# Optimization experiments

Measured on AMD Instinct MI355X. Metric: run time of the kernel, lower is better.

The kernel has to match this reference:

```python
import jax, jax.numpy as jnp
import numpy as np

EPS = 1e-5
POW = 0.5

def _eig_fun(X, fn):
    # symmetric matrix function via eigendecomposition: V f(diag) V^T
    w, V = jnp.linalg.eigh(X)
    return jnp.einsum('...ij,...j,...kj->...ik', V, fn(w), V)

def sym_pow(X, p):
    return _eig_fun(X, lambda w: jnp.power(w, p))

def sym_log(X):
    return _eig_fun(X, jnp.log)

def sym_exp(X):
    return _eig_fun(X, jnp.exp)

def exp_at(T, G):
    # Riemannian exp of tangent T at base point G (affine-invariant metric)
    Gh = sym_pow(G, 0.5)
    Gnh = sym_pow(G, -0.5)
    return Gh @ sym_exp(Gnh @ T @ Gnh) @ Gh

def bary_geom(X, n_iter=1):
    # Karcher/geodesic mean of batch of SPD matrices X: (B, n, n)
    # init at arithmetic mean, n_iter Karcher flow steps
    G = jnp.mean(X, axis=0)
    for _ in range(n_iter):
        Gh = sym_pow(G, 0.5)
        Gnh = sym_pow(G, -0.5)
        T = jnp.mean(sym_log(Gnh @ X @ Gnh), axis=0)
        G = Gh @ sym_exp(T) @ Gh
    return G

def setup_inputs() -> dict:
    key = jax.random.key(0)
    N, h, n = 256, 16, 64
    k1, k2, k3 = jax.random.split(key, 3)
    A = jax.random.normal(k1, (N, h, n, n), dtype=jnp.float32)
    # well-conditioned SPD inputs with distinct eigenvalues
    X = A @ jnp.swapaxes(A, -1, -2) / n + 0.5 * jnp.eye(n, dtype=jnp.float32)
    Bw = jax.random.normal(k2, (n, n), dtype=jnp.float32) * 0.1
    weight = sym_exp(0.5 * (Bw + Bw.T))  # SPD parameter near identity
    Bm = jax.random.normal(k3, (n, n), dtype=jnp.float32) * 0.1
    M = sym_exp(0.5 * (Bm + Bm.T))       # SPD deformation parameter
    shift = jnp.ones((1,), dtype=jnp.float32)
    return {"X": X, "weight": weight, "M": M, "shift": shift}

def reference(X, weight, M, shift):
    N, h, n, _ = X.shape
    Xb = X.reshape(N * h, n, n)
    Xp = sym_pow(Xb, POW)                  # PowerEig(X, po)
    Mnh = sym_pow(M, -0.5)
    Mh = sym_pow(M, 0.5)
    Xc = Mnh @ Xp @ Mnh                    # CongrG(., M, 'neg')
    Wp = sym_pow(weight, POW)              # PowerEig(weight, po)
    Wc = Mnh @ Wp @ Mnh                    # CongrG1(weight, M, 'neg')

    mean = bary_geom(Xc)                   # BaryGeom (training path)
    mnh = sym_pow(mean, -0.5)
    # pal1(mean, LogG(Xc, mean)) = PT of Riemannian log to identity
    T = sym_log(mnh @ Xc @ mnh)            # (N*h, n, n) tangent at I
    # cal_var: mean squared Riemannian distance to the mean
    var = jnp.mean(jnp.sum(T * T, axis=(-2, -1)))
    T = T * (shift[0] / jnp.sqrt(var + EPS))  # scale1
    Wh = sym_pow(weight, 0.5)
    S = Wh @ T @ Wh                        # pal2(weight, LogG1(.))
    Y = exp_at(S, Wc)                      # ExpG(., weight_deformed)
    Y = Mh @ Y @ Mh                        # CongrG(., M, 'pos')
    Y = sym_pow(Y, 1.0 / POW)              # PowerEig(., 1/po)
    return Y.reshape(N, h, n, n)
```

## Files before the change

### kernel.cpp

```cpp
#include <hip/hip_runtime.h>
#include <math.h>

#define PITCH 72
#define SW_BATCH 9
#define SW_SMALL 10
#define NPART 32
#define EPS2_ROT 1e-12f

#define OFF_ACCG 0
#define OFF_ACCT (NPART*4096)
#define OFF_BASE (2*NPART*4096)
#define SL_MNH  (OFF_BASE + 0*4096)
#define SL_MH   (OFF_BASE + 1*4096)
#define SL_WH   (OFF_BASE + 2*4096)
#define SL_P    (OFF_BASE + 3*4096)
#define SL_Q    (OFF_BASE + 4*4096)
#define SL_GH   (OFF_BASE + 5*4096)
#define SL_GNH  (OFF_BASE + 6*4096)
#define SL_MNH2 (OFF_BASE + 7*4096)
#define SL_WCH  (OFF_BASE + 8*4096)
#define OFF_VAR (OFF_BASE + 9*4096)
#define SL_SC   (OFF_BASE + 9*4096 + 1)

struct __align__(16) F4 { float v[4]; };

struct __align__(16) Smem {
  float S0[64*PITCH];
  float S1[64*PITCH];
  float w2[64];
  float wc[64];
  float nrm[64];
  float red[256];
  int flag;
};

__device__ __forceinline__ void g2s(float* dst, const float* __restrict__ src) {
  int t = threadIdx.x;
#pragma unroll
  for (int i = 0; i < 4; ++i) {
    int e4 = t + (i << 8);
    F4 vv = *(const F4*)&src[e4 * 4];
    *(F4*)&dst[(e4 >> 4) * PITCH + (e4 & 15) * 4] = vv;
  }
  __syncthreads();
}
__device__ __forceinline__ void g2s_scaled(float* dst, const float* __restrict__ src, float sc) {
  int t = threadIdx.x;
#pragma unroll
  for (int i = 0; i < 4; ++i) {
    int e4 = t + (i << 8);
    F4 vv = *(const F4*)&src[e4 * 4];
#pragma unroll
    for (int m = 0; m < 4; ++m) vv.v[m] *= sc;
    *(F4*)&dst[(e4 >> 4) * PITCH + (e4 & 15) * 4] = vv;
  }
  __syncthreads();
}
__device__ __forceinline__ void s2g(float* __restrict__ dst, const float* src) {
  int t = threadIdx.x;
#pragma unroll
  for (int i = 0; i < 4; ++i) {
    int e4 = t + (i << 8);
    F4 vv = *(const F4*)&src[(e4 >> 4) * PITCH + (e4 & 15) * 4];
    *(F4*)&dst[e4 * 4] = vv;
  }
  __syncthreads();
}

template<int MODE>
__device__ void mmX(Smem& sm) {
  int t = threadIdx.x;
  int R0 = t >> 4;
  if (MODE == 2) {
    int J0 = t & 15;
    float acc[4][4] = {};
    for (int kb = 0; kb < 64; kb += 4) {
      F4 a4[4];
#pragma unroll
      for (int i = 0; i < 4; ++i)
        a4[i] = *(const F4*)&sm.S0[(R0 + 16 * i) * PITCH + kb];
#pragma unroll
      for (int kk = 0; kk < 4; ++kk) {
        float b[4];
#pragma unroll
        for (int m = 0; m < 4; ++m) b[m] = sm.S1[(J0 + 16 * m) * PITCH + kb + kk];
#pragma unroll
        for (int i = 0; i < 4; ++i)
#pragma unroll
          for (int m = 0; m < 4; ++m) acc[i][m] = fmaf(a4[i].v[kk], b[m], acc[i][m]);
      }
    }
    __syncthreads();
#pragma unroll
    for (int i = 0; i < 4; ++i)
#pragma unroll
      for (int m = 0; m < 4; ++m)
        sm.S0[(R0 + 16 * i) * PITCH + J0 + 16 * m] = acc[i][m];
    __syncthreads();
  } else {
    int J = (t & 15) * 4;
    float acc[4][4] = {};
    for (int kb = 0; kb < 64; kb += 4) {
      F4 a4[4], b4[4];
#pragma unroll
      for (int i = 0; i < 4; ++i) {
        const float* L = (MODE == 0 || MODE == 3) ? sm.S1 : sm.S0;
        a4[i] = *(const F4*)&L[(R0 + 16 * i) * PITCH + kb];
      }
#pragma unroll
      for (int kk = 0; kk < 4; ++kk) {
        const float* Rp = (MODE == 0) ? sm.S0 : sm.S1;
        b4[kk] = *(const F4*)&Rp[(kb + kk) * PITCH + J];
      }
#pragma unroll
      for (int i = 0; i < 4; ++i)
#pragma unroll
        for (int kk = 0; kk < 4; ++kk)
#pragma unroll
          for (int m = 0; m < 4; ++m)
            acc[i][m] = fmaf(a4[i].v[kk], b4[kk].v[m], acc[i][m]);
    }
    __syncthreads();
#pragma unroll
    for (int i = 0; i < 4; ++i) {
      F4 o;
#pragma unroll
      for (int m = 0; m < 4; ++m) o.v[m] = acc[i][m];
      *(F4*)&sm.S0[(R0 + 16 * i) * PITCH + J] = o;
    }
    __syncthreads();
  }
}

__device__ void reconT(Smem& sm) {
  __syncthreads();
  int t = threadIdx.x;
  int R0 = t >> 4;
  int J = (t & 15) * 4;
  float acc[4][4] = {};
  for (int k = 0; k < 64; ++k) {
    float w = sm.wc[k];
    float a[4];
#pragma unroll
    for (int i = 0; i < 4; ++i) a[i] = w * sm.S0[k * PITCH + R0 + 16 * i];
    F4 b = *(const F4*)&sm.S0[k * PITCH + J];
#pragma unroll
    for (int i = 0; i < 4; ++i)
#pragma unroll
      for (int m = 0; m < 4; ++m) acc[i][m] = fmaf(a[i], b.v[m], acc[i][m]);
  }
#pragma unroll
  for (int i = 0; i < 4; ++i) {
    F4 o;
#pragma unroll
    for (int m = 0; m < 4; ++m) o.v[m] = acc[i][m];
    *(F4*)&sm.S1[(R0 + 16 * i) * PITCH + J] = o;
  }
  __syncthreads();
}

__device__ float frob2(Smem& sm) {
  int t = threadIdx.x;
  float s = 0.f;
#pragma unroll
  for (int i = 0; i < 4; ++i) {
    int e4 = t + (i << 8);
    F4 vv = *(const F4*)&sm.S0[(e4 >> 4) * PITCH + (e4 & 15) * 4];
#pragma unroll
    for (int m = 0; m < 4; ++m) s = fmaf(vv.v[m], vv.v[m], s);
  }
  sm.red[t] = s;
  __syncthreads();
  for (int o = 128; o; o >>= 1) { if (t < o) sm.red[t] += sm.red[t + o]; __syncthreads(); }
  float f = sm.red[0];
  __syncthreads();
  return f;
}

__device__ void hestenes(Smem& sm, int sweeps) {
  const int t = threadIdx.x;
  const int g = t >> 3;
  const int u = t & 7;
  float* A = sm.S0;

  {
    float sa = 0.f, sb = 0.f;
#pragma unroll
    for (int i = 0; i < 8; ++i) {
      float va = A[g * PITCH + u + 8 * i];
      float vb = A[(g + 32) * PITCH + u + 8 * i];
      sa = fmaf(va, va, sa); sb = fmaf(vb, vb, sb);
    }
    sa += __shfl_xor(sa, 1); sa += __shfl_xor(sa, 2); sa += __shfl_xor(sa, 4);
    sb += __shfl_xor(sb, 1); sb += __shfl_xor(sb, 2); sb += __shfl_xor(sb, 4);
    if (u == 0) { sm.nrm[g] = sa; sm.nrm[g + 32] = sb; }
    if (t == 0) sm.flag = 0;
  }
  __syncthreads();

  for (int s = 0; s < sweeps; ++s) {
    for (int r = 0; r < 63; ++r) {
      int p, q;
      if (g == 0) { p = 63; q = r; }
      else {
        int a = r + g;      if (a >= 63) a -= 63;
        int b = r + 63 - g; if (b >= 63) b -= 63;
        p = a; q = b;
      }
      const int bp = p * PITCH + u, bq = q * PITCH + u;
      float cp[8], cq[8];
#pragma unroll
      for (int i = 0; i < 8; ++i) { cp[i] = A[bp + 8 * i]; cq[i] = A[bq + 8 * i]; }
      float d = 0.f;
#pragma unroll
      for (int i = 0; i < 8; ++i) d = fmaf(cp[i], cq[i], d);
      d += __shfl_xor(d, 1); d += __shfl_xor(d, 2); d += __shfl_xor(d, 4);
      float dpp = sm.nrm[p], dqq = sm.nrm[q];
      if (d * d > EPS2_ROT * (dpp * dqq)) {
        float tau = (dqq - dpp) * (0.5f * __builtin_amdgcn_rcpf(d));
        float tt = __builtin_amdgcn_rcpf(fabsf(tau) +
                                         __builtin_amdgcn_sqrtf(fmaf(tau, tau, 1.f)));
        if (tau < 0.f) tt = -tt;
        float c = __builtin_amdgcn_rsqf(fmaf(tt, tt, 1.f));
        float s_ = tt * c;
#pragma unroll
        for (int i = 0; i < 8; ++i) {
          A[bp + 8 * i] = c * cp[i] - s_ * cq[i];
          A[bq + 8 * i] = s_ * cp[i] + c * cq[i];
        }
        if (u == 0) {
          float td = tt * d;
          sm.nrm[p] = dpp - td;
          sm.nrm[q] = dqq + td;
          sm.flag = 1;
        }
      }
      __syncthreads();
    }
    int f = sm.flag;
    __syncthreads();
    if (f == 0) break;
    if (t == 0) sm.flag = 0;
    __syncthreads();
  }

  {
    float sa = 0.f, sb = 0.f;
#pragma unroll
    for (int i = 0; i < 8; ++i) {
      float va = A[g * PITCH + u + 8 * i];
      float vb = A[(g + 32) * PITCH + u + 8 * i];
      sa = fmaf(va, va, sa); sb = fmaf(vb, vb, sb);
    }
    sa += __shfl_xor(sa, 1); sa += __shfl_xor(sa, 2); sa += __shfl_xor(sa, 4);
    sb += __shfl_xor(sb, 1); sb += __shfl_xor(sb, 2); sb += __shfl_xor(sb, 4);
    if (u == 0) { sm.w2[g] = sa; sm.w2[g + 32] = sb; }
  }
  __syncthreads();
}


__global__ __launch_bounds__(256) void kzero(float* ws) {
  int i = blockIdx.x * 256 + threadIdx.x;
  if (i < OFF_BASE) ws[i] = 0.f;
  if (i == 0) ws[OFF_VAR] = 0.f;
}

__global__ __launch_bounds__(256, 4) void kprep(const float* __restrict__ weight,
                                                const float* __restrict__ M,
                                                float* ws) {
  __shared__ Smem sm;
  int t = threadIdx.x;
  g2s(sm.S0, M);
  hestenes(sm, SW_SMALL);
  if (t < 64) sm.wc[t] = powf(fmaxf(sm.w2[t], 1e-12f), -1.25f);
  reconT(sm); s2g(ws + SL_MNH, sm.S1);
  if (t < 64) sm.wc[t] = powf(fmaxf(sm.w2[t], 1e-12f), -0.75f);
  reconT(sm); s2g(ws + SL_MH, sm.S1);

  g2s(sm.S0, weight);
  hestenes(sm, SW_SMALL);
  if (t < 64) sm.wc[t] = powf(fmaxf(sm.w2[t], 1e-12f), -0.75f);
  reconT(sm); s2g(ws + SL_WH, sm.S1);

  g2s(sm.S0, ws + SL_MNH);
  mmX<1>(sm);
  g2s(sm.S1, ws + SL_MNH);
  mmX<1>(sm);
  hestenes(sm, SW_SMALL);
  if (t < 64) sm.wc[t] = powf(fmaxf(sm.w2[t], 1e-12f), -0.75f);
  reconT(sm); s2g(ws + SL_WCH, sm.S1);
  if (t < 64) sm.wc[t] = powf(fmaxf(sm.w2[t], 1e-12f), -1.25f);
  reconT(sm);
  g2s(sm.S0, ws + SL_WH);
  mmX<0>(sm);
  s2g(ws + SL_P, sm.S0);
  g2s(sm.S0, ws + SL_WCH);
  g2s(sm.S1, ws + SL_MH);
  mmX<0>(sm);
  s2g(ws + SL_Q, sm.S0);
}

__global__ __launch_bounds__(256, 4) void k1(const float* __restrict__ X,
                                             float* __restrict__ out, float* ws) {
  __shared__ Smem sm;
  int t = threadIdx.x;
  size_t b = blockIdx.x;
  g2s(sm.S0, X + b * 4096);
  hestenes(sm, SW_BATCH);
  g2s(sm.S1, ws + SL_MNH);
  mmX<1>(sm);
  if (t < 64) sm.wc[t] = powf(fmaxf(sm.w2[t], 1e-12f), -0.75f);
  reconT(sm);
  float* Xc = out + b * 4096;
  float* acc = ws + OFF_ACCG + (size_t)(blockIdx.x & (NPART - 1)) * 4096;
#pragma unroll
  for (int i = 0; i < 4; ++i) {
    int e4 = t + (i << 8);
    F4 vv = *(const F4*)&sm.S1[(e4 >> 4) * PITCH + (e4 & 15) * 4];
    *(F4*)&Xc[e4 * 4] = vv;
#pragma unroll
    for (int m = 0; m < 4; ++m) atomicAdd(acc + e4 * 4 + m, vv.v[m]);
  }
}

__global__ __launch_bounds__(256, 4) void ksmall2(float* ws, float invB) {
  __shared__ Smem sm;
  int t = threadIdx.x;
#pragma unroll
  for (int i = 0; i < 4; ++i) {
    int e4 = t + (i << 8);
    F4 sum = {{0.f, 0.f, 0.f, 0.f}};
    for (int p = 0; p < NPART; ++p) {
      F4 vv = *(const F4*)&ws[OFF_ACCG + p * 4096 + e4 * 4];
#pragma unroll
      for (int m = 0; m < 4; ++m) sum.v[m] += vv.v[m];
    }
#pragma unroll
    for (int m = 0; m < 4; ++m) sum.v[m] *= invB;
    *(F4*)&sm.S0[(e4 >> 4) * PITCH + (e4 & 15) * 4] = sum;
  }
  __syncthreads();
  hestenes(sm, SW_SMALL);
  if (t < 64) sm.wc[t] = powf(fmaxf(sm.w2[t], 1e-12f), -0.75f);
  reconT(sm); s2g(ws + SL_GH, sm.S1);
  if (t < 64) sm.wc[t] = powf(fmaxf(sm.w2[t], 1e-12f), -1.25f);
  reconT(sm); s2g(ws + SL_GNH, sm.S1);
}

__global__ __launch_bounds__(256, 4) void k2(const float* __restrict__ XcBuf, float* ws) {
  __shared__ Smem sm;
  int t = threadIdx.x;
  size_t b = blockIdx.x;
  g2s(sm.S0, XcBuf + b * 4096);
  g2s(sm.S1, ws + SL_GNH);
  mmX<1>(sm);
  mmX<0>(sm);
  hestenes(sm, SW_BATCH);
  if (t < 64) {
    float s2 = fmaxf(sm.w2[t], 1e-12f);
    sm.wc[t] = 0.5f * logf(s2) / s2;
  }
  reconT(sm);
  float* acc = ws + OFF_ACCT + (size_t)(blockIdx.x & (NPART - 1)) * 4096;
#pragma unroll
  for (int i = 0; i < 4; ++i) {
    int e4 = t + (i << 8);
    F4 vv = *(const F4*)&sm.S1[(e4 >> 4) * PITCH + (e4 & 15) * 4];
#pragma unroll
    for (int m = 0; m < 4; ++m) atomicAdd(acc + e4 * 4 + m, vv.v[m]);
  }
}

__global__ __launch_bounds__(256, 4) void ksmall3(float* ws, float invB) {
  __shared__ Smem sm;
  int t = threadIdx.x;
#pragma unroll
  for (int i = 0; i < 4; ++i) {
    int e4 = t + (i << 8);
    F4 sum = {{0.f, 0.f, 0.f, 0.f}};
    for (int p = 0; p < NPART; ++p) {
      F4 vv = *(const F4*)&ws[OFF_ACCT + p * 4096 + e4 * 4];
#pragma unroll
      for (int m = 0; m < 4; ++m) sum.v[m] += vv.v[m];
    }
#pragma unroll
    for (int m = 0; m < 4; ++m) sum.v[m] *= invB;
    *(F4*)&sm.S0[(e4 >> 4) * PITCH + (e4 & 15) * 4] = sum;
  }
  __syncthreads();
  float mu = sqrtf(frob2(sm)) + 1e-3f;
  if (t < 64) sm.S0[t * PITCH + t] += mu;
  __syncthreads();
  hestenes(sm, SW_SMALL);
  if (t < 64) {
    float s2 = fmaxf(sm.w2[t], 1e-12f);
    sm.wc[t] = expf(sqrtf(s2) - mu) / s2;
  }
  reconT(sm);
  g2s(sm.S0, ws + SL_GH);
  mmX<1>(sm);
  g2s(sm.S1, ws + SL_GH);
  mmX<1>(sm);
  hestenes(sm, SW_SMALL);
  if (t < 64) sm.wc[t] = powf(fmaxf(sm.w2[t], 1e-12f), -1.25f);
  reconT(sm); s2g(ws + SL_MNH2, sm.S1);
}

__global__ __launch_bounds__(256, 4) void k3(float* __restrict__ buf, float* ws) {
  __shared__ Smem sm;
  int t = threadIdx.x;
  size_t b = blockIdx.x;
  g2s(sm.S0, buf + b * 4096);
  g2s(sm.S1, ws + SL_MNH2);
  mmX<1>(sm);
  mmX<0>(sm);
  hestenes(sm, SW_BATCH);
  if (t < 64) {
    float s2 = fmaxf(sm.w2[t], 1e-12f);
    sm.wc[t] = 0.5f * logf(s2) / s2;
  }
  reconT(sm);
  float ssq = 0.f;
  float* Tg = buf + b * 4096;
#pragma unroll
  for (int i = 0; i < 4; ++i) {
    int e4 = t + (i << 8);
    F4 vv = *(const F4*)&sm.S1[(e4 >> 4) * PITCH + (e4 & 15) * 4];
    *(F4*)&Tg[e4 * 4] = vv;
#pragma unroll
    for (int m = 0; m < 4; ++m) ssq = fmaf(vv.v[m], vv.v[m], ssq);
  }
  sm.red[t] = ssq;
  __syncthreads();
  for (int o = 128; o; o >>= 1) { if (t < o) sm.red[t] += sm.red[t + o]; __syncthreads(); }
  if (t == 0) atomicAdd(ws + OFF_VAR, sm.red[0]);
}

__global__ void kscale(float* ws, const float* __restrict__ shift, float invB) {
  if (threadIdx.x == 0 && blockIdx.x == 0) {
    float var = ws[OFF_VAR] * invB;
    ws[SL_SC] = shift[0] / sqrtf(var + 1e-5f);
  }
}

__global__ __launch_bounds__(256, 4) void k4(float* __restrict__ buf, float* ws) {
  __shared__ Smem sm;
  int t = threadIdx.x;
  size_t b = blockIdx.x;
  float sc = ws[SL_SC];
  g2s_scaled(sm.S0, buf + b * 4096, sc);
  g2s(sm.S1, ws + SL_P);
  mmX<0>(sm);
  mmX<2>(sm);
  float mu = sqrtf(frob2(sm)) + 1e-3f;
  if (t < 64) sm.S0[t * PITCH + t] += mu;
  __syncthreads();
  hestenes(sm, SW_BATCH);
  if (t < 64) {
    float s2 = fmaxf(sm.w2[t], 1e-12f);
    sm.wc[t] = expf(sqrtf(s2) - mu) / s2;
  }
  g2s(sm.S1, ws + SL_Q);
  mmX<2>(sm);
  reconT(sm);
  mmX<3>(sm);
  s2g(buf + b * 4096, sm.S0);
}

extern "C" void kernel_launch(void* const* d_in, const int* in_sizes, int n_in,
                              void* d_out, int out_size, void* d_ws, size_t ws_size,
                              hipStream_t stream) {
  const float* X      = (const float*)d_in[0];
  const float* weight = (const float*)d_in[1];
  const float* M      = (const float*)d_in[2];
  const float* shift  = (const float*)d_in[3];
  float* out = (float*)d_out;
  float* ws  = (float*)d_ws;
  int B = in_sizes[0] / 4096;
  float invB = 1.f / (float)B;

  hipLaunchKernelGGL(kzero,   dim3(OFF_BASE / 256), dim3(256), 0, stream, ws);
  hipLaunchKernelGGL(kprep,   dim3(1), dim3(256), 0, stream, weight, M, ws);
  hipLaunchKernelGGL(k1,      dim3(B), dim3(256), 0, stream, X, out, ws);
  hipLaunchKernelGGL(ksmall2, dim3(1), dim3(256), 0, stream, ws, invB);
  hipLaunchKernelGGL(k2,      dim3(B), dim3(256), 0, stream, out, ws);
  hipLaunchKernelGGL(ksmall3, dim3(1), dim3(256), 0, stream, ws, invB);
  hipLaunchKernelGGL(k3,      dim3(B), dim3(256), 0, stream, out, ws);
  hipLaunchKernelGGL(kscale,  dim3(1), dim3(64), 0, stream, ws, shift, invB);
  hipLaunchKernelGGL(k4,      dim3(B), dim3(256), 0, stream, out, ws);
}
```

Before: 9.694 ms.

## Run one-sided Jacobi per wavefront in registers, four matrices per block

Replaces the block-wide shared-memory Hestenes Jacobi with a register-resident version. Each 64-lane wavefront owns one matrix, one column per lane, and exchanges columns with xor shuffles in a round-robin pairing, so the per-rotation __syncthreads and LDS traffic go away. Each block now processes four matrices, and the batched kernels (k1-k4) are relaunched with B/4 blocks and a smaller shared pitch. The cost is heavy register pressure (64+64 floats per lane, occupancy hint lowered to 3), fewer blocks, and a higher sweep cap (12 vs 9) that may add iterations before convergence.

After: 9.168 ms. 5.4% less time.

```diff
diff --git a/kernel.cpp b/kernel.cpp
--- a/kernel.cpp
+++ b/kernel.cpp
@@ -2,7 +2,8 @@
 #include <math.h>
 
 #define PITCH 72
-#define SW_BATCH 9
+#define NP 68
+#define SW_BATCH 12
 #define SW_SMALL 10
 #define NPART 32
 #define EPS2_ROT 1e-12f
@@ -44,18 +45,6 @@
   }
   __syncthreads();
 }
-__device__ __forceinline__ void g2s_scaled(float* dst, const float* __restrict__ src, float sc) {
-  int t = threadIdx.x;
-#pragma unroll
-  for (int i = 0; i < 4; ++i) {
-    int e4 = t + (i << 8);
-    F4 vv = *(const F4*)&src[e4 * 4];
-#pragma unroll
-    for (int m = 0; m < 4; ++m) vv.v[m] *= sc;
-    *(F4*)&dst[(e4 >> 4) * PITCH + (e4 & 15) * 4] = vv;
-  }
-  __syncthreads();
-}
 __device__ __forceinline__ void s2g(float* __restrict__ dst, const float* src) {
   int t = threadIdx.x;
 #pragma unroll
@@ -71,65 +60,37 @@
 __device__ void mmX(Smem& sm) {
   int t = threadIdx.x;
   int R0 = t >> 4;
-  if (MODE == 2) {
-    int J0 = t & 15;
-    float acc[4][4] = {};
-    for (int kb = 0; kb < 64; kb += 4) {
-      F4 a4[4];
-#pragma unroll
-      for (int i = 0; i < 4; ++i)
-        a4[i] = *(const F4*)&sm.S0[(R0 + 16 * i) * PITCH + kb];
-#pragma unroll
-      for (int kk = 0; kk < 4; ++kk) {
-        float b[4];
-#pragma unroll
-        for (int m = 0; m < 4; ++m) b[m] = sm.S1[(J0 + 16 * m) * PITCH + kb + kk];
-#pragma unroll
-        for (int i = 0; i < 4; ++i)
-#pragma unroll
-          for (int m = 0; m < 4; ++m) acc[i][m] = fmaf(a4[i].v[kk], b[m], acc[i][m]);
-      }
-    }
-    __syncthreads();
+  int J = (t & 15) * 4;
+  float acc[4][4] = {};
+  for (int kb = 0; kb < 64; kb += 4) {
+    F4 a4[4], b4[4];
+#pragma unroll
+    for (int i = 0; i < 4; ++i) {
+      const float* L = (MODE == 0) ? sm.S1 : sm.S0;
+      a4[i] = *(const F4*)&L[(R0 + 16 * i) * PITCH + kb];
+    }
+#pragma unroll
+    for (int kk = 0; kk < 4; ++kk) {
+      const float* Rp = (MODE == 0) ? sm.S0 : sm.S1;
+      b4[kk] = *(const F4*)&Rp[(kb + kk) * PITCH + J];
+    }
 #pragma unroll
     for (int i = 0; i < 4; ++i)
 #pragma unroll
-      for (int m = 0; m < 4; ++m)
-        sm.S0[(R0 + 16 * i) * PITCH + J0 + 16 * m] = acc[i][m];
-    __syncthreads();
-  } else {
-    int J = (t & 15) * 4;
-    float acc[4][4] = {};
-    for (int kb = 0; kb < 64; kb += 4) {
-      F4 a4[4], b4[4];
-#pragma unroll
-      for (int i = 0; i < 4; ++i) {
-        const float* L = (MODE == 0 || MODE == 3) ? sm.S1 : sm.S0;
-        a4[i] = *(const F4*)&L[(R0 + 16 * i) * PITCH + kb];
-      }
-#pragma unroll
-      for (int kk = 0; kk < 4; ++kk) {
-        const float* Rp = (MODE == 0) ? sm.S0 : sm.S1;
-        b4[kk] = *(const F4*)&Rp[(kb + kk) * PITCH + J];
-      }
-#pragma unroll
-      for (int i = 0; i < 4; ++i)
-#pragma unroll
-        for (int kk = 0; kk < 4; ++kk)
-#pragma unroll
-          for (int m = 0; m < 4; ++m)
-            acc[i][m] = fmaf(a4[i].v[kk], b4[kk].v[m], acc[i][m]);
-    }
-    __syncthreads();
-#pragma unroll
-    for (int i = 0; i < 4; ++i) {
-      F4 o;
-#pragma unroll
-      for (int m = 0; m < 4; ++m) o.v[m] = acc[i][m];
-      *(F4*)&sm.S0[(R0 + 16 * i) * PITCH + J] = o;
-    }
-    __syncthreads();
-  }
+      for (int kk = 0; kk < 4; ++kk)
+#pragma unroll
+        for (int m = 0; m < 4; ++m)
+          acc[i][m] = fmaf(a4[i].v[kk], b4[kk].v[m], acc[i][m]);
+  }
+  __syncthreads();
+#pragma unroll
+  for (int i = 0; i < 4; ++i) {
+    F4 o;
+#pragma unroll
+    for (int m = 0; m < 4; ++m) o.v[m] = acc[i][m];
+    *(F4*)&sm.S0[(R0 + 16 * i) * PITCH + J] = o;
+  }
+  __syncthreads();
 }
 
 __device__ void reconT(Smem& sm) {
@@ -182,7 +143,6 @@
   const int g = t >> 3;
   const int u = t & 7;
   float* A = sm.S0;
-
   {
     float sa = 0.f, sb = 0.f;
 #pragma unroll
@@ -257,6 +217,201 @@
     if (u == 0) { sm.w2[g] = sa; sm.w2[g + 32] = sb; }
   }
   __syncthreads();
+}
+
+struct __align__(16) SmemK {
+  float A[64*NP];
+  float Bop[64*NP];
+  float wc[64];
+  float red[256];
+};
+struct __align__(16) SmemK4 {
+  float A[64*NP];
+  float P[64*NP];
+  float Q[64*NP];
+  float wc[64];
+  float red[256];
+};
+
+__device__ __forceinline__ void g2s68(float* dst, const float* __restrict__ src) {
+  int t = threadIdx.x;
+#pragma unroll
+  for (int i = 0; i < 4; ++i) {
+    int e4 = t + (i << 8);
+    F4 vv = *(const F4*)&src[e4 * 4];
+    *(F4*)&dst[(e4 >> 4) * NP + (e4 & 15) * 4] = vv;
+  }
+  __syncthreads();
+}
+__device__ __forceinline__ void g2s68s(float* dst, const float* __restrict__ src, float sc) {
+  int t = threadIdx.x;
+#pragma unroll
+  for (int i = 0; i < 4; ++i) {
+    int e4 = t + (i << 8);
+    F4 vv = *(const F4*)&src[e4 * 4];
+#pragma unroll
+    for (int m = 0; m < 4; ++m) vv.v[m] *= sc;
+    *(F4*)&dst[(e4 >> 4) * NP + (e4 & 15) * 4] = vv;
+  }
+  __syncthreads();
+}
+
+template<int MODE>
+__device__ void mm68(float* A, const float* Bo) {
+  int t = threadIdx.x;
+  int R0 = t >> 4;
+  if (MODE == 2) {
+    int J0 = t & 15;
+    float acc[4][4] = {};
+    for (int kb = 0; kb < 64; kb += 4) {
+      F4 a4[4];
+#pragma unroll
+      for (int i = 0; i < 4; ++i) a4[i] = *(const F4*)&A[(R0 + 16 * i) * NP + kb];
+#pragma unroll
+      for (int kk = 0; kk < 4; ++kk) {
+        float b[4];
+#pragma unroll
+        for (int m = 0; m < 4; ++m) b[m] = Bo[(J0 + 16 * m) * NP + kb + kk];
+#pragma unroll
+        for (int i = 0; i < 4; ++i)
+#pragma unroll
+          for (int m = 0; m < 4; ++m) acc[i][m] = fmaf(a4[i].v[kk], b[m], acc[i][m]);
+      }
+    }
+    __syncthreads();
+#pragma unroll
+    for (int i = 0; i < 4; ++i)
+#pragma unroll
+      for (int m = 0; m < 4; ++m)
+        A[(R0 + 16 * i) * NP + J0 + 16 * m] = acc[i][m];
+    __syncthreads();
+  } else {
+    int J = (t & 15) * 4;
+    float acc[4][4] = {};
+    for (int kb = 0; kb < 64; kb += 4) {
+      F4 a4[4], b4[4];
+#pragma unroll
+      for (int i = 0; i < 4; ++i) {
+        const float* L = (MODE == 0) ? Bo : A;
+        a4[i] = *(const F4*)&L[(R0 + 16 * i) * NP + kb];
+      }
+#pragma unroll
+      for (int kk = 0; kk < 4; ++kk) {
+        const float* Rp = (MODE == 0) ? A : Bo;
+        b4[kk] = *(const F4*)&Rp[(kb + kk) * NP + J];
+      }
+#pragma unroll
+      for (int i = 0; i < 4; ++i)
+#pragma unroll
+        for (int kk = 0; kk < 4; ++kk)
+#pragma unroll
+          for (int m = 0; m < 4; ++m)
+            acc[i][m] = fmaf(a4[i].v[kk], b4[kk].v[m], acc[i][m]);
+    }
+    __syncthreads();
+#pragma unroll
+    for (int i = 0; i < 4; ++i) {
+      F4 o;
+#pragma unroll
+      for (int m = 0; m < 4; ++m) o.v[m] = acc[i][m];
+      *(F4*)&A[(R0 + 16 * i) * NP + J] = o;
+    }
+    __syncthreads();
+  }
+}
+
+__device__ float frob68(const float* A, float* red) {
+  int t = threadIdx.x;
+  float s = 0.f;
+#pragma unroll
+  for (int i = 0; i < 4; ++i) {
+    int e4 = t + (i << 8);
+    F4 vv = *(const F4*)&A[(e4 >> 4) * NP + (e4 & 15) * 4];
+#pragma unroll
+    for (int m = 0; m < 4; ++m) s = fmaf(vv.v[m], vv.v[m], s);
+  }
+  red[t] = s;
+  __syncthreads();
+  for (int o = 128; o; o >>= 1) { if (t < o) red[t] += red[t + o]; __syncthreads(); }
+  float f = red[0];
+  __syncthreads();
+  return f;
+}
+
+__device__ void msq_store(const float* Z, float* __restrict__ gout) {
+  int t = threadIdx.x;
+  int R0 = t >> 4;
+  int J = (t & 15) * 4;
+  float acc[4][4] = {};
+  for (int kb = 0; kb < 64; kb += 4) {
+    F4 a4[4], b4[4];
+#pragma unroll
+    for (int i = 0; i < 4; ++i) a4[i] = *(const F4*)&Z[(R0 + 16 * i) * NP + kb];
+#pragma unroll
+    for (int kk = 0; kk < 4; ++kk) b4[kk] = *(const F4*)&Z[(kb + kk) * NP + J];
+#pragma unroll
+    for (int i = 0; i < 4; ++i)
+#pragma unroll
+      for (int kk = 0; kk < 4; ++kk)
+#pragma unroll
+        for (int m = 0; m < 4; ++m)
+          acc[i][m] = fmaf(a4[i].v[kk], b4[kk].v[m], acc[i][m]);
+  }
+#pragma unroll
+  for (int i = 0; i < 4; ++i) {
+    F4 o;
+#pragma unroll
+    for (int m = 0; m < 4; ++m) o.v[m] = acc[i][m];
+    *(F4*)&gout[(R0 + 16 * i) * 64 + J] = o;
+  }
+}
+
+__device__ __forceinline__ void hestenes_reg(float (&own)[64], float& w2out, int sweeps) {
+  const int lane = threadIdx.x & 63;
+  float nrm = 0.f;
+#pragma unroll
+  for (int i = 0; i < 64; ++i) nrm = fmaf(own[i], own[i], nrm);
+
+  for (int s = 0; s < sweeps; ++s) {
+    bool any = false;
+    for (int m = 1; m < 64; ++m) {
+      float pv[64];
+#pragma unroll
+      for (int i = 0; i < 64; ++i) pv[i] = __shfl_xor(own[i], m);
+      float d0 = 0.f, d1 = 0.f, d2 = 0.f, d3 = 0.f;
+#pragma unroll
+      for (int i = 0; i < 64; i += 4) {
+        d0 = fmaf(own[i + 0], pv[i + 0], d0);
+        d1 = fmaf(own[i + 1], pv[i + 1], d1);
+        d2 = fmaf(own[i + 2], pv[i + 2], d2);
+        d3 = fmaf(own[i + 3], pv[i + 3], d3);
+      }
+      float d = (d0 + d1) + (d2 + d3);
+      float pn = __shfl_xor(nrm, m);
+      if (d * d > EPS2_ROT * (nrm * pn)) {
+        any = true;
+        bool lo = lane < (lane ^ m);
+        float dpp = lo ? nrm : pn;
+        float dqq = lo ? pn : nrm;
+        float tau = (dqq - dpp) * (0.5f * __builtin_amdgcn_rcpf(d));
+        float tt = __builtin_amdgcn_rcpf(fabsf(tau) +
+                                         __builtin_amdgcn_sqrtf(fmaf(tau, tau, 1.f)));
+        if (tau < 0.f) tt = -tt;
+        float c = __builtin_amdgcn_rsqf(fmaf(tt, tt, 1.f));
+        float s_ = tt * c;
+        float sg = lo ? -s_ : s_;
+#pragma unroll
+        for (int i = 0; i < 64; ++i) own[i] = fmaf(sg, pv[i], c * own[i]);
+        float td = tt * d;
+        nrm += lo ? -td : td;
+      }
+    }
+    if (!__any((int)any)) break;
+  }
+  float w = 0.f;
+#pragma unroll
+  for (int i = 0; i < 64; ++i) w = fmaf(own[i], own[i], w);
+  w2out = w;
 }
 
 
@@ -301,26 +456,64 @@
   s2g(ws + SL_Q, sm.S0);
 }
 
-__global__ __launch_bounds__(256, 4) void k1(const float* __restrict__ X,
+__global__ __launch_bounds__(256, 3) void k1(const float* __restrict__ X,
                                              float* __restrict__ out, float* ws) {
-  __shared__ Smem sm;
-  int t = threadIdx.x;
+  __shared__ SmemK sm;
+  int t = threadIdx.x;
+  int w = t >> 6, lane = t & 63;
   size_t b = blockIdx.x;
-  g2s(sm.S0, X + b * 4096);
-  hestenes(sm, SW_BATCH);
-  g2s(sm.S1, ws + SL_MNH);
-  mmX<1>(sm);
-  if (t < 64) sm.wc[t] = powf(fmaxf(sm.w2[t], 1e-12f), -0.75f);
-  reconT(sm);
-  float* Xc = out + b * 4096;
-  float* acc = ws + OFF_ACCG + (size_t)(blockIdx.x & (NPART - 1)) * 4096;
-#pragma unroll
-  for (int i = 0; i < 4; ++i) {
-    int e4 = t + (i << 8);
-    F4 vv = *(const F4*)&sm.S1[(e4 >> 4) * PITCH + (e4 & 15) * 4];
-    *(F4*)&Xc[e4 * 4] = vv;
-#pragma unroll
-    for (int m = 0; m < 4; ++m) atomicAdd(acc + e4 * 4 + m, vv.v[m]);
+  g2s68(sm.Bop, ws + SL_MNH);
+
+  float own[64]; float w2;
+  {
+    const float* Xm = X + (b * 4 + w) * 4096 + (size_t)lane * 64;
+#pragma unroll
+    for (int j = 0; j < 16; ++j) {
+      F4 r = *(const F4*)&Xm[4 * j];
+      own[4 * j + 0] = r.v[0]; own[4 * j + 1] = r.v[1];
+      own[4 * j + 2] = r.v[2]; own[4 * j + 3] = r.v[3];
+    }
+  }
+  hestenes_reg(own, w2, SW_BATCH);
+  __syncthreads();
+
+  int R0 = t >> 4, J = (t & 15) * 4;
+  for (int m = 0; m < 4; ++m) {
+    if (w == m) {
+#pragma unroll
+      for (int j = 0; j < 16; ++j) {
+        F4 o = {{own[4 * j], own[4 * j + 1], own[4 * j + 2], own[4 * j + 3]}};
+        *(F4*)&sm.A[lane * NP + 4 * j] = o;
+      }
+      sm.wc[lane] = powf(fmaxf(w2, 1e-12f), -0.75f);
+    }
+    __syncthreads();
+    mm68<1>(sm.A, sm.Bop);
+    float acc[4][4] = {};
+    for (int k = 0; k < 64; ++k) {
+      float wck = sm.wc[k];
+      float a[4];
+#pragma unroll
+      for (int i = 0; i < 4; ++i) a[i] = wck * sm.A[k * NP + R0 + 16 * i];
+      F4 bb = *(const F4*)&sm.A[k * NP + J];
+#pragma unroll
+      for (int i = 0; i < 4; ++i)
+#pragma unroll
+        for (int mc = 0; mc < 4; ++mc) acc[i][mc] = fmaf(a[i], bb.v[mc], acc[i][mc]);
+    }
+    float* Xc = out + (b * 4 + m) * 4096;
+    float* accp = ws + OFF_ACCG + (size_t)((b * 4 + m) & (NPART - 1)) * 4096;
+#pragma unroll
+    for (int i = 0; i < 4; ++i) {
+      F4 o;
+#pragma unroll
+      for (int mc = 0; mc < 4; ++mc) o.v[mc] = acc[i][mc];
+      int base = (R0 + 16 * i) * 64 + J;
+      *(F4*)&Xc[base] = o;
+#pragma unroll
+      for (int mc = 0; mc < 4; ++mc) atomicAdd(accp + base + mc, o.v[mc]);
+    }
+    __syncthreads();
   }
 }
 
@@ -348,27 +541,59 @@
   reconT(sm); s2g(ws + SL_GNH, sm.S1);
 }
 
-__global__ __launch_bounds__(256, 4) void k2(const float* __restrict__ XcBuf, float* ws) {
-  __shared__ Smem sm;
-  int t = threadIdx.x;
+__global__ __launch_bounds__(256, 3) void k2(const float* __restrict__ XcBuf, float* ws) {
+  __shared__ SmemK sm;
+  int t = threadIdx.x;
+  int w = t >> 6, lane = t & 63;
   size_t b = blockIdx.x;
-  g2s(sm.S0, XcBuf + b * 4096);
-  g2s(sm.S1, ws + SL_GNH);
-  mmX<1>(sm);
-  mmX<0>(sm);
-  hestenes(sm, SW_BATCH);
-  if (t < 64) {
-    float s2 = fmaxf(sm.w2[t], 1e-12f);
-    sm.wc[t] = 0.5f * logf(s2) / s2;
-  }
-  reconT(sm);
-  float* acc = ws + OFF_ACCT + (size_t)(blockIdx.x & (NPART - 1)) * 4096;
-#pragma unroll
-  for (int i = 0; i < 4; ++i) {
-    int e4 = t + (i << 8);
-    F4 vv = *(const F4*)&sm.S1[(e4 >> 4) * PITCH + (e4 & 15) * 4];
-#pragma unroll
-    for (int m = 0; m < 4; ++m) atomicAdd(acc + e4 * 4 + m, vv.v[m]);
+  g2s68(sm.Bop, ws + SL_GNH);
+
+  float own[64]; float w2;
+  for (int m = 0; m < 4; ++m) {
+    g2s68(sm.A, XcBuf + (b * 4 + m) * 4096);
+    mm68<1>(sm.A, sm.Bop);
+    mm68<0>(sm.A, sm.Bop);
+    if (w == m) {
+#pragma unroll
+      for (int i = 0; i < 64; ++i) own[i] = sm.A[i * NP + lane];
+    }
+    __syncthreads();
+  }
+  hestenes_reg(own, w2, SW_BATCH);
+  __syncthreads();
+
+  int R0 = t >> 4, J = (t & 15) * 4;
+  for (int m = 0; m < 4; ++m) {
+    if (w == m) {
+#pragma unroll
+      for (int j = 0; j < 16; ++j) {
+        F4 o = {{own[4 * j], own[4 * j + 1], own[4 * j + 2], own[4 * j + 3]}};
+        *(F4*)&sm.A[lane * NP + 4 * j] = o;
+      }
+      float s2 = fmaxf(w2, 1e-12f);
+      sm.wc[lane] = 0.5f * logf(s2) / s2;
+    }
+    __syncthreads();
+    float acc[4][4] = {};
+    for (int k = 0; k < 64; ++k) {
+      float wck = sm.wc[k];
+      float a[4];
+#pragma unroll
+      for (int i = 0; i < 4; ++i) a[i] = wck * sm.A[k * NP + R0 + 16 * i];
+      F4 bb = *(const F4*)&sm.A[k * NP + J];
+#pragma unroll
+      for (int i = 0; i < 4; ++i)
+#pragma unroll
+        for (int mc = 0; mc < 4; ++mc) acc[i][mc] = fmaf(a[i], bb.v[mc], acc[i][mc]);
+    }
+    float* accp = ws + OFF_ACCT + (size_t)((b * 4 + m) & (NPART - 1)) * 4096;
+#pragma unroll
+    for (int i = 0; i < 4; ++i) {
+      int base = (R0 + 16 * i) * 64 + J;
+#pragma unroll
+      for (int mc = 0; mc < 4; ++mc) atomicAdd(accp + base + mc, acc[i][mc]);
+    }
+    __syncthreads();
   }
 }
 
@@ -407,34 +632,69 @@
   reconT(sm); s2g(ws + SL_MNH2, sm.S1);
 }
 
-__global__ __launch_bounds__(256, 4) void k3(float* __restrict__ buf, float* ws) {
-  __shared__ Smem sm;
-  int t = threadIdx.x;
+__global__ __launch_bounds__(256, 3) void k3(float* __restrict__ buf, float* ws) {
+  __shared__ SmemK sm;
+  int t = threadIdx.x;
+  int w = t >> 6, lane = t & 63;
   size_t b = blockIdx.x;
-  g2s(sm.S0, buf + b * 4096);
-  g2s(sm.S1, ws + SL_MNH2);
-  mmX<1>(sm);
-  mmX<0>(sm);
-  hestenes(sm, SW_BATCH);
-  if (t < 64) {
-    float s2 = fmaxf(sm.w2[t], 1e-12f);
-    sm.wc[t] = 0.5f * logf(s2) / s2;
-  }
-  reconT(sm);
-  float ssq = 0.f;
-  float* Tg = buf + b * 4096;
-#pragma unroll
-  for (int i = 0; i < 4; ++i) {
-    int e4 = t + (i << 8);
-    F4 vv = *(const F4*)&sm.S1[(e4 >> 4) * PITCH + (e4 & 15) * 4];
-    *(F4*)&Tg[e4 * 4] = vv;
-#pragma unroll
-    for (int m = 0; m < 4; ++m) ssq = fmaf(vv.v[m], vv.v[m], ssq);
-  }
-  sm.red[t] = ssq;
-  __syncthreads();
-  for (int o = 128; o; o >>= 1) { if (t < o) sm.red[t] += sm.red[t + o]; __syncthreads(); }
-  if (t == 0) atomicAdd(ws + OFF_VAR, sm.red[0]);
+  g2s68(sm.Bop, ws + SL_MNH2);
+
+  float own[64]; float w2;
+  for (int m = 0; m < 4; ++m) {
+    g2s68(sm.A, buf + (b * 4 + m) * 4096);
+    mm68<1>(sm.A, sm.Bop);
+    mm68<0>(sm.A, sm.Bop);
+    if (w == m) {
+#pragma unroll
+      for (int i = 0; i < 64; ++i) own[i] = sm.A[i * NP + lane];
+    }
+    __syncthreads();
+  }
+  hestenes_reg(own, w2, SW_BATCH);
+  __syncthreads();
+
+  int R0 = t >> 4, J = (t & 15) * 4;
+  for (int m = 0; m < 4; ++m) {
+    if (w == m) {
+#pragma unroll
+      for (int j = 0; j < 16; ++j) {
+        F4 o = {{own[4 * j], own[4 * j + 1], own[4 * j + 2], own[4 * j + 3]}};
+        *(F4*)&sm.A[lane * NP + 4 * j] = o;
+      }
+      float s2 = fmaxf(w2, 1e-12f);
+      sm.wc[lane] = 0.5f * logf(s2) / s2;
+    }
+    __syncthreads();
+    float acc[4][4] = {};
+    for (int k = 0; k < 64; ++k) {
+      float wck = sm.wc[k];
+      float a[4];
+#pragma unroll
+      for (int i = 0; i < 4; ++i) a[i] = wck * sm.A[k * NP + R0 + 16 * i];
+      F4 bb = *(const F4*)&sm.A[k * NP + J];
+#pragma unroll
+      for (int i = 0; i < 4; ++i)
+#pragma unroll
+        for (int mc = 0; mc < 4; ++mc) acc[i][mc] = fmaf(a[i], bb.v[mc], acc[i][mc]);
+    }
+    float* Tg = buf + (b * 4 + m) * 4096;
+    float ssq = 0.f;
+#pragma unroll
+    for (int i = 0; i < 4; ++i) {
+      F4 o;
+#pragma unroll
+      for (int mc = 0; mc < 4; ++mc) o.v[mc] = acc[i][mc];
+      int base = (R0 + 16 * i) * 64 + J;
+      *(F4*)&Tg[base] = o;
+#pragma unroll
+      for (int mc = 0; mc < 4; ++mc) ssq = fmaf(o.v[mc], o.v[mc], ssq);
+    }
+    sm.red[t] = ssq;
+    __syncthreads();
+    for (int o = 128; o; o >>= 1) { if (t < o) sm.red[t] += sm.red[t + o]; __syncthreads(); }
+    if (t == 0) atomicAdd(ws + OFF_VAR, sm.red[0]);
+    __syncthreads();
+  }
 }
 
 __global__ void kscale(float* ws, const float* __restrict__ shift, float invB) {
@@ -444,28 +704,70 @@
   }
 }
 
-__global__ __launch_bounds__(256, 4) void k4(float* __restrict__ buf, float* ws) {
-  __shared__ Smem sm;
-  int t = threadIdx.x;
+__global__ __launch_bounds__(256, 3) void k4(float* __restrict__ buf, float* ws) {
+  __shared__ SmemK4 sm;
+  int t = threadIdx.x;
+  int w = t >> 6, lane = t & 63;
   size_t b = blockIdx.x;
   float sc = ws[SL_SC];
-  g2s_scaled(sm.S0, buf + b * 4096, sc);
-  g2s(sm.S1, ws + SL_P);
-  mmX<0>(sm);
-  mmX<2>(sm);
-  float mu = sqrtf(frob2(sm)) + 1e-3f;
-  if (t < 64) sm.S0[t * PITCH + t] += mu;
-  __syncthreads();
-  hestenes(sm, SW_BATCH);
-  if (t < 64) {
-    float s2 = fmaxf(sm.w2[t], 1e-12f);
-    sm.wc[t] = expf(sqrtf(s2) - mu) / s2;
-  }
-  g2s(sm.S1, ws + SL_Q);
-  mmX<2>(sm);
-  reconT(sm);
-  mmX<3>(sm);
-  s2g(buf + b * 4096, sm.S0);
+  g2s68(sm.P, ws + SL_P);
+  g2s68(sm.Q, ws + SL_Q);
+
+  float own[64]; float w2; float muw = 0.f;
+  for (int m = 0; m < 4; ++m) {
+    g2s68s(sm.A, buf + (b * 4 + m) * 4096, sc);
+    mm68<0>(sm.A, sm.P);
+    mm68<2>(sm.A, sm.P);
+    float f = frob68(sm.A, sm.red);
+    if (w == m) {
+      muw = sqrtf(f) + 1e-3f;
+#pragma unroll
+      for (int i = 0; i < 64; ++i) {
+        float v = sm.A[i * NP + lane];
+        own[i] = v + ((i == lane) ? muw : 0.f);
+      }
+    }
+    __syncthreads();
+  }
+  hestenes_reg(own, w2, SW_BATCH);
+  __syncthreads();
+
+  int R0 = t >> 4, J = (t & 15) * 4;
+  for (int m = 0; m < 4; ++m) {
+    if (w == m) {
+#pragma unroll
+      for (int j = 0; j < 16; ++j) {
+        F4 o = {{own[4 * j], own[4 * j + 1], own[4 * j + 2], own[4 * j + 3]}};
+        *(F4*)&sm.A[lane * NP + 4 * j] = o;
+      }
+      float s2 = fmaxf(w2, 1e-12f);
+      sm.wc[lane] = expf(sqrtf(s2) - muw) / s2;
+    }
+    __syncthreads();
+    mm68<2>(sm.A, sm.Q);
+    float acc[4][4] = {};
+    for (int k = 0; k < 64; ++k) {
+      float wck = sm.wc[k];
+      float a[4];
+#pragma unroll
+      for (int i = 0; i < 4; ++i) a[i] = wck * sm.A[k * NP + R0 + 16 * i];
+      F4 bb = *(const F4*)&sm.A[k * NP + J];
+#pragma unroll
+      for (int i = 0; i < 4; ++i)
+#pragma unroll
+        for (int mc = 0; mc < 4; ++mc) acc[i][mc] = fmaf(a[i], bb.v[mc], acc[i][mc]);
+    }
+#pragma unroll
+    for (int i = 0; i < 4; ++i) {
+      F4 o;
+#pragma unroll
+      for (int mc = 0; mc < 4; ++mc) o.v[mc] = acc[i][mc];
+      *(F4*)&sm.P[(R0 + 16 * i) * NP + J] = o;
+    }
+    __syncthreads();
+    msq_store(sm.P, buf + (b * 4 + m) * 4096);
+    __syncthreads();
+  }
 }
 
 extern "C" void kernel_launch(void* const* d_in, const int* in_sizes, int n_in,
@@ -479,14 +781,15 @@
   float* ws  = (float*)d_ws;
   int B = in_sizes[0] / 4096;
   float invB = 1.f / (float)B;
+  int G = B / 4;
 
   hipLaunchKernelGGL(kzero,   dim3(OFF_BASE / 256), dim3(256), 0, stream, ws);
   hipLaunchKernelGGL(kprep,   dim3(1), dim3(256), 0, stream, weight, M, ws);
-  hipLaunchKernelGGL(k1,      dim3(B), dim3(256), 0, stream, X, out, ws);
+  hipLaunchKernelGGL(k1,      dim3(G), dim3(256), 0, stream, X, out, ws);
   hipLaunchKernelGGL(ksmall2, dim3(1), dim3(256), 0, stream, ws, invB);
-  hipLaunchKernelGGL(k2,      dim3(B), dim3(256), 0, stream, out, ws);
+  hipLaunchKernelGGL(k2,      dim3(G), dim3(256), 0, stream, out, ws);
   hipLaunchKernelGGL(ksmall3, dim3(1), dim3(256), 0, stream, ws, invB);
-  hipLaunchKernelGGL(k3,      dim3(B), dim3(256), 0, stream, out, ws);
+  hipLaunchKernelGGL(k3,      dim3(G), dim3(256), 0, stream, out, ws);
   hipLaunchKernelGGL(kscale,  dim3(1), dim3(64), 0, stream, ws, shift, invB);
-  hipLaunchKernelGGL(k4,      dim3(B), dim3(256), 0, stream, out, ws);
-}
+  hipLaunchKernelGGL(k4,      dim3(G), dim3(256), 0, stream, out, ws);
+}
```
